# Optimization experiments

Hardware: AMD Instinct MI355X
Metric: run time of the kernel (lower is better)

Reference implementation:

```python
import jax, jax.numpy as jnp
import numpy as np

N_USERS = 200000
N_SPOTS = 50000
N_EDGES = 3200000
D = 64


def setup_inputs() -> dict:
    key = jax.random.key(0)
    k1, k2, k3, k4 = jax.random.split(key, 4)
    return {
        "user_x": jax.random.normal(k1, (N_USERS, D), dtype=jnp.float32),
        "spot_x": jax.random.normal(k2, (N_SPOTS, D), dtype=jnp.float32),
        "user_idx": jax.random.randint(k3, (N_EDGES,), 0, N_USERS, dtype=jnp.int32),
        "spot_idx": jax.random.randint(k4, (N_EDGES,), 0, N_SPOTS, dtype=jnp.int32),
    }


def reference(user_x, spot_x, user_idx, spot_idx):
    n_users, n_spots = user_x.shape[0], spot_x.shape[0]
    dtype = user_x.dtype
    ones = jnp.ones(user_idx.shape[0], dtype=dtype)
    # per-node degrees (counts of edge endpoints); isolated nodes get 1e-6
    user_div = jax.ops.segment_sum(ones, user_idx, num_segments=n_users)
    spot_div = jax.ops.segment_sum(ones, spot_idx, num_segments=n_spots)
    user_div = jnp.where(user_div == 0, jnp.asarray(1e-6, dtype), user_div)
    spot_div = jnp.where(spot_div == 0, jnp.asarray(1e-6, dtype), spot_div)
    inv_sqrt_user = jax.lax.rsqrt(user_div)  # [n_users]
    inv_sqrt_spot = jax.lax.rsqrt(spot_div)  # [n_spots]
    # gather + pre-normalize per-edge messages
    spot_msg = spot_x[spot_idx] * inv_sqrt_spot[spot_idx][:, None]  # [E, D]
    user_msg = user_x[user_idx] * inv_sqrt_user[user_idx][:, None]  # [E, D]
    # scatter-add into destination nodes, then post-normalize by dest degree
    spot_out = jax.ops.segment_sum(user_msg, spot_idx, num_segments=n_spots)
    user_out = jax.ops.segment_sum(spot_msg, user_idx, num_segments=n_users)
    spot_out = spot_out * inv_sqrt_spot[:, None]
    user_out = user_out * inv_sqrt_user[:, None]
    return (user_out, spot_out)
```

## Files before the change

### kernel.cpp

```cpp
#include <hip/hip_runtime.h>
#include <hip/hip_fp16.h>

#define DFEAT  64
#define BSH    7
#define BN     128
#define PBITS  18
#define PMASK  ((1u << PBITS) - 1)
#define NSPLIT 384
#define STR_U  2560
#define STR_S  9216

typedef float          __attribute__((ext_vector_type(4))) f32x4;
typedef unsigned short __attribute__((ext_vector_type(4))) u16x4;


__device__ __forceinline__ long long bucket_base(int b, int NB_U) {
    return (b < NB_U) ? (long long)b * STR_U
                      : (long long)NB_U * STR_U + (long long)(b - NB_U) * STR_S;
}

__global__ __launch_bounds__(256) void split_kernel(const int* __restrict__ uidx,
                                                    const int* __restrict__ sidx,
                                                    int* __restrict__ cursor,
                                                    unsigned int* __restrict__ staging,
                                                    int n_edges, int NB_U, int NB) {
    __shared__ int h[2048];
    __shared__ int rc[2048];
    for (int i = threadIdx.x; i < NB; i += 256) h[i] = 0;
    __syncthreads();
    int epb = (((n_edges + gridDim.x - 1) / gridDim.x) + 3) & ~3;
    int e0 = blockIdx.x * epb;
    int e1 = min(e0 + epb, n_edges);
    int len = e1 - e0; if (len < 0) len = 0;
    int nv = e0 + (len & ~3);
    for (int v = e0 + 4 * (int)threadIdx.x; v < nv; v += 1024) {
        int4 u = *(const int4*)(uidx + v);
        int4 s = *(const int4*)(sidx + v);
        atomicAdd(&h[u.x >> BSH], 1); atomicAdd(&h[u.y >> BSH], 1);
        atomicAdd(&h[u.z >> BSH], 1); atomicAdd(&h[u.w >> BSH], 1);
        atomicAdd(&h[NB_U + (s.x >> BSH)], 1); atomicAdd(&h[NB_U + (s.y >> BSH)], 1);
        atomicAdd(&h[NB_U + (s.z >> BSH)], 1); atomicAdd(&h[NB_U + (s.w >> BSH)], 1);
    }
    for (int e = nv + (int)threadIdx.x; e < e1; e += 256) {
        atomicAdd(&h[uidx[e] >> BSH], 1);
        atomicAdd(&h[NB_U + (sidx[e] >> BSH)], 1);
    }
    __syncthreads();
    for (int i = threadIdx.x; i < NB; i += 256) {
        int c = h[i];
        rc[i] = c ? (int)(bucket_base(i, NB_U) + atomicAdd(&cursor[i], c)) : 0;
    }
    __syncthreads();
    for (int v = e0 + 4 * (int)threadIdx.x; v < nv; v += 1024) {
        int4 u4 = *(const int4*)(uidx + v);
        int4 s4 = *(const int4*)(sidx + v);
#pragma unroll
        for (int k = 0; k < 4; ++k) {
            int u = ((const int*)&u4)[k];
            int s = ((const int*)&s4)[k];
            int pu = atomicAdd(&rc[u >> BSH], 1);
            staging[pu] = ((unsigned int)(u & (BN - 1)) << PBITS) | (unsigned int)s;
            int ps = atomicAdd(&rc[NB_U + (s >> BSH)], 1);
            staging[ps] = ((unsigned int)(s & (BN - 1)) << PBITS) | (unsigned int)u;
        }
    }
    for (int e = nv + (int)threadIdx.x; e < e1; e += 256) {
        int u = uidx[e], s = sidx[e];
        int pu = atomicAdd(&rc[u >> BSH], 1);
        staging[pu] = ((unsigned int)(u & (BN - 1)) << PBITS) | (unsigned int)s;
        int ps = atomicAdd(&rc[NB_U + (s >> BSH)], 1);
        staging[ps] = ((unsigned int)(s & (BN - 1)) << PBITS) | (unsigned int)u;
    }
}

template <int CAPN>
__global__ __launch_bounds__(256) void csr_build_inplace_t(
        unsigned int* __restrict__ staging,
        const int* __restrict__ cursor,
        int* __restrict__ start,
        int* __restrict__ cnt,
        float* __restrict__ isq,
        const float* __restrict__ ux,
        const float* __restrict__ sx,
        unsigned short* __restrict__ scaledH,
        int n_users, int n_spots,
        int NB_U, int b0) {
    __shared__ unsigned int buf[CAPN];
    __shared__ int hist[BN];
    __shared__ int scanbuf[BN];
    __shared__ int cur[BN];
    __shared__ float fisq[BN];
    int b = b0 + blockIdx.x, t = threadIdx.x;
    long long beg = bucket_base(b, NB_U);
    int len = cursor[b];
    if (len > CAPN) len = CAPN;
    if (t < BN) hist[t] = 0;
    __syncthreads();
    for (int i = t; i < len; i += 256) {
        unsigned int e = __builtin_nontemporal_load(&staging[beg + i]);
        buf[i] = e;
        atomicAdd(&hist[e >> PBITS], 1);
    }
    __syncthreads();
    if (t < BN) scanbuf[t] = hist[t];
    __syncthreads();
    for (int off = 1; off < BN; off <<= 1) {
        int v = (t >= off && t < BN) ? scanbuf[t - off] : 0;
        __syncthreads();
        if (t < BN) scanbuf[t] += v;
        __syncthreads();
    }
    bool ub = (b < NB_U);
    int node0 = (ub ? (b << BSH) : ((b - NB_U) << BSH));
    int lim   = ub ? n_users : n_spots;
    if (t < BN) {
        int excl = scanbuf[t] - hist[t];
        cur[t] = (int)beg + excl;
        int node = node0 + t;
        if (node < lim) {
            int gi = ub ? node : (n_users + node);
            start[gi] = (int)beg + excl;
            cnt[gi]   = hist[t];
            float d = hist[t] ? (float)hist[t] : 1e-6f;
            float is = rsqrtf(d);
            isq[gi]  = is;
            fisq[t]  = is;
        }
    }
    __syncthreads();
    for (int i = t; i < len; i += 256) {
        unsigned int e = buf[i];
        int pos = atomicAdd(&cur[e >> PBITS], 1);
        staging[pos] = e & PMASK;
    }
    const f32x4* __restrict__ xs4 = (const f32x4*)(ub ? ux : sx);
    u16x4* __restrict__ dst4 = (u16x4*)scaledH + ((long long)(ub ? node0 : n_users + node0) << 4);
#pragma unroll
    for (int k = 0; k < 8; ++k) {
        int idx4 = t + k * 256;
        int nl = idx4 >> 4;
        int node = node0 + nl;
        if (node < lim) {
            f32x4 v = __builtin_nontemporal_load(xs4 + ((long long)node << 4) + (idx4 & 15));
            float f = fisq[nl];
            u16x4 hh;
            hh.x = __half_as_ushort(__float2half(v.x * f));
            hh.y = __half_as_ushort(__float2half(v.y * f));
            hh.z = __half_as_ushort(__float2half(v.z * f));
            hh.w = __half_as_ushort(__float2half(v.w * f));
            dst4[((long long)nl << 4) + (idx4 & 15)] = hh;
        }
    }
}

template <int G>
__device__ __forceinline__ void gather_groupH(int j, int pv,
        const unsigned short* __restrict__ src, int lane,
        float& a0, float& a1, float& a2, float& a3) {
    unsigned short v[G];
#pragma unroll
    for (int k = 0; k < G; ++k) {
        int p = __builtin_amdgcn_readlane(pv, j + k);
        v[k] = src[(p << 6) + lane];
    }
    __builtin_amdgcn_sched_barrier(0);
#pragma unroll
    for (int k = 0; k < G; ++k) {
        float x = __half2float(__ushort_as_half(v[k]));
        if ((k & 3) == 0) a0 += x;
        else if ((k & 3) == 1) a1 += x;
        else if ((k & 3) == 2) a2 += x;
        else a3 += x;
    }
}

__global__ __launch_bounds__(256) void gather_h(
        const unsigned short* __restrict__ scaled,
        const float* __restrict__ isq,
        const int* __restrict__ start,
        const int* __restrict__ cnt,
        const int* __restrict__ csr,
        float* __restrict__ user_out,
        float* __restrict__ spot_out,
        int n_users, int n_spots) {
    int lane = (int)threadIdx.x & 63;
    int w = __builtin_amdgcn_readfirstlane((int)blockIdx.x * 4 + ((int)threadIdx.x >> 6));
    int A = n_users + n_spots;
    if (w >= A) return;
    bool ub = (w < n_users);
    const unsigned short* __restrict__ src =
        scaled + (ub ? ((long long)n_users << 6) : 0);
    int beg = __builtin_amdgcn_readfirstlane(start[w]);
    int end = beg + __builtin_amdgcn_readfirstlane(cnt[w]);
    float a0 = 0.f, a1 = 0.f, a2 = 0.f, a3 = 0.f;
    for (int i = beg; i < end; i += 64) {
        int n = end - i; if (n > 64) n = 64;
        int pv = 0;
        if (lane < n) pv = __builtin_nontemporal_load(&csr[i + lane]);
        int j = 0;
        for (; j + 16 <= n; j += 16)
            gather_groupH<16>(j, pv, src, lane, a0, a1, a2, a3);
        if (j + 8 <= n) { gather_groupH<8>(j, pv, src, lane, a0, a1, a2, a3); j += 8; }
        if (j + 4 <= n) { gather_groupH<4>(j, pv, src, lane, a0, a1, a2, a3); j += 4; }
        for (; j < n; ++j) {
            int p = __builtin_amdgcn_readlane(pv, j);
            a0 += __half2float(__ushort_as_half(src[(p << 6) + lane]));
        }
    }
    float r = ((a0 + a1) + (a2 + a3)) * isq[w];
    if (ub) __builtin_nontemporal_store(r, &user_out[((long long)w << 6) + lane]);
    else    __builtin_nontemporal_store(r, &spot_out[((long long)(w - n_users) << 6) + lane]);
}


__global__ void deg_kernel(const int* __restrict__ uidx,
                           const int* __restrict__ sidx,
                           unsigned int* __restrict__ udeg,
                           unsigned int* __restrict__ sdeg,
                           int n_edges) {
    int e = blockIdx.x * blockDim.x + threadIdx.x;
    if (e < n_edges) {
        atomicAdd(&udeg[uidx[e]], 1u);
        atomicAdd(&sdeg[sidx[e]], 1u);
    }
}

__global__ void rsqrt_kernel(unsigned int* __restrict__ deg_as_uint,
                             float* __restrict__ isq, int n) {
    int i = blockIdx.x * blockDim.x + threadIdx.x;
    if (i < n) {
        float d = (float)deg_as_uint[i];
        if (d == 0.0f) d = 1e-6f;
        isq[i] = rsqrtf(d);
    }
}

__global__ void scatter_kernel(const float* __restrict__ user_x,
                               const float* __restrict__ spot_x,
                               const int* __restrict__ uidx,
                               const int* __restrict__ sidx,
                               const float* __restrict__ isqu,
                               const float* __restrict__ isqs,
                               float* __restrict__ user_out,
                               float* __restrict__ spot_out,
                               int n_edges) {
    long long t = (long long)blockIdx.x * blockDim.x + threadIdx.x;
    int e = (int)(t >> 6);
    int lane = (int)(t & 63);
    if (e < n_edges) {
        int u = uidx[e];
        int s = sidx[e];
        float sv = spot_x[(long long)s * DFEAT + lane] * isqs[s];
        float uv = user_x[(long long)u * DFEAT + lane] * isqu[u];
        unsafeAtomicAdd(&user_out[(long long)u * DFEAT + lane], sv);
        unsafeAtomicAdd(&spot_out[(long long)s * DFEAT + lane], uv);
    }
}

__global__ void scale_kernel(float* __restrict__ user_out,
                             float* __restrict__ spot_out,
                             const float* __restrict__ isqu,
                             const float* __restrict__ isqs,
                             int n_users, int n_spots) {
    long long t = (long long)blockIdx.x * blockDim.x + threadIdx.x;
    long long total_u = (long long)n_users * DFEAT;
    long long total_s = (long long)n_spots * DFEAT;
    if (t < total_u) {
        user_out[t] *= isqu[t >> 6];
    } else if (t < total_u + total_s) {
        long long t2 = t - total_u;
        spot_out[t2] *= isqs[t2 >> 6];
    }
}


extern "C" void kernel_launch(void* const* d_in, const int* in_sizes, int n_in,
                              void* d_out, int out_size, void* d_ws, size_t ws_size,
                              hipStream_t stream) {
    const float* user_x = (const float*)d_in[0];
    const float* spot_x = (const float*)d_in[1];
    const int* uidx = (const int*)d_in[2];
    const int* sidx = (const int*)d_in[3];

    const int n_users = in_sizes[0] / DFEAT;
    const int n_spots = in_sizes[1] / DFEAT;
    const int n_edges = in_sizes[2];
    const int A = n_users + n_spots;

    float* user_out = (float*)d_out;
    float* spot_out = (float*)d_out + (long long)n_users * DFEAT;

    const int NB_U = (n_users + BN - 1) / BN;
    const int NB_S = (n_spots + BN - 1) / BN;
    const int NB = NB_U + NB_S;

    const long long SE = (long long)NB_U * STR_U + (long long)NB_S * STR_S;
    const long long off_start = NB;
    const long long off_cnt   = off_start + A;
    const long long off_isq   = off_cnt + A;
    const long long off_stg   = off_isq + A;
    const long long off_scl   = (off_stg + SE + 1) & ~1LL;
    const long long need = off_scl * 4 + (long long)A * DFEAT * 2;

    bool fits = NB <= 2048 &&
                n_users <= (1 << PBITS) && n_spots <= (1 << PBITS);

    if (fits && (long long)ws_size >= need) {
        int* cursor           = (int*)d_ws;
        int* start            = (int*)d_ws + off_start;
        int* cnt              = (int*)d_ws + off_cnt;
        float* isq            = (float*)d_ws + off_isq;
        unsigned int* staging = (unsigned int*)d_ws + off_stg;
        unsigned short* scaledH = (unsigned short*)((int*)d_ws + off_scl);

        hipMemsetAsync(cursor, 0, (size_t)NB * 4, stream);

        split_kernel<<<NSPLIT, 256, 0, stream>>>(uidx, sidx, cursor, staging,
                                                 n_edges, NB_U, NB);
        csr_build_inplace_t<STR_S><<<NB_S, 256, 0, stream>>>(
            staging, cursor, start, cnt, isq, user_x, spot_x, scaledH,
            n_users, n_spots, NB_U, NB_U);
        csr_build_inplace_t<STR_U><<<NB_U, 256, 0, stream>>>(
            staging, cursor, start, cnt, isq, user_x, spot_x, scaledH,
            n_users, n_spots, NB_U, 0);
        {
            long long total = (long long)A * 64;
            int blocks = (int)((total + 255) / 256);
            gather_h<<<blocks, 256, 0, stream>>>(
                scaledH, isq, start, cnt, (const int*)staging,
                user_out, spot_out, n_users, n_spots);
        }
    } else {
        float* isqu = (float*)d_ws;
        float* isqs = isqu + n_users;
        unsigned int* udeg = (unsigned int*)isqu;
        unsigned int* sdeg = (unsigned int*)isqs;

        hipMemsetAsync(d_out, 0, (size_t)out_size * sizeof(float), stream);
        hipMemsetAsync(d_ws, 0, (size_t)A * sizeof(unsigned int), stream);

        {
            int blocks = (n_edges + 255) / 256;
            deg_kernel<<<blocks, 256, 0, stream>>>(uidx, sidx, udeg, sdeg, n_edges);
        }
        {
            int blocks = (A + 255) / 256;
            rsqrt_kernel<<<blocks, 256, 0, stream>>>((unsigned int*)d_ws, (float*)d_ws, A);
        }
        {
            long long total = (long long)n_edges * 64;
            int blocks = (int)((total + 255) / 256);
            scatter_kernel<<<blocks, 256, 0, stream>>>(
                user_x, spot_x, uidx, sidx, isqu, isqs, user_out, spot_out, n_edges);
        }
        {
            long long total = (long long)A * 64;
            int blocks = (int)((total + 255) / 256);
            scale_kernel<<<blocks, 256, 0, stream>>>(
                user_out, spot_out, isqu, isqs, n_users, n_spots);
        }
    }
}
```

Before: 429.5 us.

## Shrink spot buckets to 32 nodes and sub-sort neighbors by coarse index bits

Spot buckets now hold 32 nodes instead of 128, so every bucket uses one uniform stride and the large 9216-entry shared buffer for spot buckets goes away. The sort key inside each bucket also carries high bits of the neighbor index (1 bit for user rows, 3 bits for spot rows), which orders each node's adjacency list into coarse neighbor ranges. The aim is higher occupancy in the CSR build and better gather locality in the later aggregation. The cost is more buckets, more split-histogram shared memory (MAXNB) and a 256-bin scan per block.

```diff
diff --git a/kernel.cpp b/kernel.cpp
--- a/kernel.cpp
+++ b/kernel.cpp
@@ -2,30 +2,26 @@
 #include <hip/hip_fp16.h>
 
 #define DFEAT  64
-#define BSH    7
-#define BN     128
+#define BSH_U  7
+#define BSH_S  5
 #define PBITS  18
 #define PMASK  ((1u << PBITS) - 1)
 #define NSPLIT 384
-#define STR_U  2560
-#define STR_S  9216
+#define STR    2560
+#define MAXNB  3328
 
 typedef float          __attribute__((ext_vector_type(4))) f32x4;
 typedef unsigned short __attribute__((ext_vector_type(4))) u16x4;
 
 
-__device__ __forceinline__ long long bucket_base(int b, int NB_U) {
-    return (b < NB_U) ? (long long)b * STR_U
-                      : (long long)NB_U * STR_U + (long long)(b - NB_U) * STR_S;
-}
-
 __global__ __launch_bounds__(256) void split_kernel(const int* __restrict__ uidx,
                                                     const int* __restrict__ sidx,
-                                                    int* __restrict__ cursor,
+                                                    int* __restrict__ bcursor,
                                                     unsigned int* __restrict__ staging,
-                                                    int n_edges, int NB_U, int NB) {
-    __shared__ int h[2048];
-    __shared__ int rc[2048];
+                                                    int n_edges, int NB_U, int NB,
+                                                    int shs, int shu) {
+    __shared__ int h[MAXNB];
+    __shared__ int rc[MAXNB];
     for (int i = threadIdx.x; i < NB; i += 256) h[i] = 0;
     __syncthreads();
     int epb = (((n_edges + gridDim.x - 1) / gridDim.x) + 3) & ~3;
@@ -36,19 +32,19 @@
     for (int v = e0 + 4 * (int)threadIdx.x; v < nv; v += 1024) {
         int4 u = *(const int4*)(uidx + v);
         int4 s = *(const int4*)(sidx + v);
-        atomicAdd(&h[u.x >> BSH], 1); atomicAdd(&h[u.y >> BSH], 1);
-        atomicAdd(&h[u.z >> BSH], 1); atomicAdd(&h[u.w >> BSH], 1);
-        atomicAdd(&h[NB_U + (s.x >> BSH)], 1); atomicAdd(&h[NB_U + (s.y >> BSH)], 1);
-        atomicAdd(&h[NB_U + (s.z >> BSH)], 1); atomicAdd(&h[NB_U + (s.w >> BSH)], 1);
+        atomicAdd(&h[u.x >> BSH_U], 1); atomicAdd(&h[u.y >> BSH_U], 1);
+        atomicAdd(&h[u.z >> BSH_U], 1); atomicAdd(&h[u.w >> BSH_U], 1);
+        atomicAdd(&h[NB_U + (s.x >> BSH_S)], 1); atomicAdd(&h[NB_U + (s.y >> BSH_S)], 1);
+        atomicAdd(&h[NB_U + (s.z >> BSH_S)], 1); atomicAdd(&h[NB_U + (s.w >> BSH_S)], 1);
     }
     for (int e = nv + (int)threadIdx.x; e < e1; e += 256) {
-        atomicAdd(&h[uidx[e] >> BSH], 1);
-        atomicAdd(&h[NB_U + (sidx[e] >> BSH)], 1);
+        atomicAdd(&h[uidx[e] >> BSH_U], 1);
+        atomicAdd(&h[NB_U + (sidx[e] >> BSH_S)], 1);
     }
     __syncthreads();
     for (int i = threadIdx.x; i < NB; i += 256) {
         int c = h[i];
-        rc[i] = c ? (int)(bucket_base(i, NB_U) + atomicAdd(&cursor[i], c)) : 0;
+        rc[i] = c ? (int)((long long)i * STR + atomicAdd(&bcursor[i], c)) : 0;
     }
     __syncthreads();
     for (int v = e0 + 4 * (int)threadIdx.x; v < nv; v += 1024) {
@@ -58,43 +54,46 @@
         for (int k = 0; k < 4; ++k) {
             int u = ((const int*)&u4)[k];
             int s = ((const int*)&s4)[k];
-            int pu = atomicAdd(&rc[u >> BSH], 1);
-            staging[pu] = ((unsigned int)(u & (BN - 1)) << PBITS) | (unsigned int)s;
-            int ps = atomicAdd(&rc[NB_U + (s >> BSH)], 1);
-            staging[ps] = ((unsigned int)(s & (BN - 1)) << PBITS) | (unsigned int)u;
+            unsigned int ku = ((unsigned int)(u & 127) << 1) | (unsigned int)(s >> shs);
+            int pu = atomicAdd(&rc[u >> BSH_U], 1);
+            staging[pu] = (ku << PBITS) | (unsigned int)s;
+            unsigned int ks = ((unsigned int)(s & 31) << 3) | (unsigned int)(u >> shu);
+            int ps = atomicAdd(&rc[NB_U + (s >> BSH_S)], 1);
+            staging[ps] = (ks << PBITS) | (unsigned int)u;
         }
     }
     for (int e = nv + (int)threadIdx.x; e < e1; e += 256) {
         int u = uidx[e], s = sidx[e];
-        int pu = atomicAdd(&rc[u >> BSH], 1);
-        staging[pu] = ((unsigned int)(u & (BN - 1)) << PBITS) | (unsigned int)s;
-        int ps = atomicAdd(&rc[NB_U + (s >> BSH)], 1);
-        staging[ps] = ((unsigned int)(s & (BN - 1)) << PBITS) | (unsigned int)u;
-    }
-}
-
-template <int CAPN>
-__global__ __launch_bounds__(256) void csr_build_inplace_t(
+        unsigned int ku = ((unsigned int)(u & 127) << 1) | (unsigned int)(s >> shs);
+        int pu = atomicAdd(&rc[u >> BSH_U], 1);
+        staging[pu] = (ku << PBITS) | (unsigned int)s;
+        unsigned int ks = ((unsigned int)(s & 31) << 3) | (unsigned int)(u >> shu);
+        int ps = atomicAdd(&rc[NB_U + (s >> BSH_S)], 1);
+        staging[ps] = (ks << PBITS) | (unsigned int)u;
+    }
+}
+
+template <int RB, int BNODES, bool UB>
+__global__ __launch_bounds__(256) void csr_build_t(
         unsigned int* __restrict__ staging,
-        const int* __restrict__ cursor,
+        const int* __restrict__ bcursor,
         int* __restrict__ start,
         int* __restrict__ cnt,
         float* __restrict__ isq,
         const float* __restrict__ ux,
         const float* __restrict__ sx,
         unsigned short* __restrict__ scaledH,
-        int n_users, int n_spots,
-        int NB_U, int b0) {
-    __shared__ unsigned int buf[CAPN];
-    __shared__ int hist[BN];
-    __shared__ int scanbuf[BN];
-    __shared__ int cur[BN];
-    __shared__ float fisq[BN];
+        int n_users, int n_spots, int NB_U, int b0) {
+    __shared__ unsigned int buf[STR];
+    __shared__ int hist[256];
+    __shared__ int scanbuf[256];
+    __shared__ int cur[256];
+    __shared__ float fisq[BNODES];
+    constexpr int NSH = (BNODES == 128) ? 7 : 5;
     int b = b0 + blockIdx.x, t = threadIdx.x;
-    long long beg = bucket_base(b, NB_U);
-    int len = cursor[b];
-    if (len > CAPN) len = CAPN;
-    if (t < BN) hist[t] = 0;
+    long long beg = (long long)b * STR;
+    int len = bcursor[b]; if (len > STR) len = STR;
+    hist[t] = 0;
     __syncthreads();
     for (int i = t; i < len; i += 256) {
         unsigned int e = __builtin_nontemporal_load(&staging[beg + i]);
@@ -102,30 +101,32 @@
         atomicAdd(&hist[e >> PBITS], 1);
     }
     __syncthreads();
-    if (t < BN) scanbuf[t] = hist[t];
-    __syncthreads();
-    for (int off = 1; off < BN; off <<= 1) {
-        int v = (t >= off && t < BN) ? scanbuf[t - off] : 0;
+    scanbuf[t] = hist[t];
+    __syncthreads();
+    for (int off = 1; off < 256; off <<= 1) {
+        int v = (t >= off) ? scanbuf[t - off] : 0;
         __syncthreads();
-        if (t < BN) scanbuf[t] += v;
+        scanbuf[t] += v;
         __syncthreads();
     }
-    bool ub = (b < NB_U);
-    int node0 = (ub ? (b << BSH) : ((b - NB_U) << BSH));
-    int lim   = ub ? n_users : n_spots;
-    if (t < BN) {
-        int excl = scanbuf[t] - hist[t];
-        cur[t] = (int)beg + excl;
+    cur[t] = (int)beg + scanbuf[t] - hist[t];
+    int node0 = UB ? (b << NSH) : ((b - NB_U) << NSH);
+    int lim   = UB ? n_users : n_spots;
+    if (t < BNODES) {
+        int fb = t << RB, lb = ((t + 1) << RB) - 1;
+        int excl0 = scanbuf[fb] - hist[fb];
+        int c = scanbuf[lb] - excl0;
         int node = node0 + t;
+        float is = 0.f;
         if (node < lim) {
-            int gi = ub ? node : (n_users + node);
-            start[gi] = (int)beg + excl;
-            cnt[gi]   = hist[t];
-            float d = hist[t] ? (float)hist[t] : 1e-6f;
-            float is = rsqrtf(d);
-            isq[gi]  = is;
-            fisq[t]  = is;
-        }
+            int gi = UB ? node : (n_users + node);
+            start[gi] = (int)beg + excl0;
+            cnt[gi]   = c;
+            float d = c ? (float)c : 1e-6f;
+            is = rsqrtf(d);
+            isq[gi] = is;
+        }
+        fisq[t] = is;
     }
     __syncthreads();
     for (int i = t; i < len; i += 256) {
@@ -133,10 +134,12 @@
         int pos = atomicAdd(&cur[e >> PBITS], 1);
         staging[pos] = e & PMASK;
     }
-    const f32x4* __restrict__ xs4 = (const f32x4*)(ub ? ux : sx);
-    u16x4* __restrict__ dst4 = (u16x4*)scaledH + ((long long)(ub ? node0 : n_users + node0) << 4);
+    const f32x4* __restrict__ xs4 = (const f32x4*)(UB ? ux : sx);
+    long long gbase = UB ? (long long)node0 : (long long)(n_users + node0);
+    u16x4* __restrict__ dst4 = (u16x4*)scaledH + (gbase << 4);
+    constexpr int ITER = (BNODES << 4) / 256;
 #pragma unroll
-    for (int k = 0; k < 8; ++k) {
+    for (int k = 0; k < ITER; ++k) {
         int idx4 = t + k * 256;
         int nl = idx4 >> 4;
         int node = node0 + nl;
@@ -290,11 +293,14 @@
     float* user_out = (float*)d_out;
     float* spot_out = (float*)d_out + (long long)n_users * DFEAT;
 
-    const int NB_U = (n_users + BN - 1) / BN;
-    const int NB_S = (n_spots + BN - 1) / BN;
+    const int NB_U = (n_users + 127) >> BSH_U;
+    const int NB_S = (n_spots + 31) >> BSH_S;
     const int NB = NB_U + NB_S;
 
-    const long long SE = (long long)NB_U * STR_U + (long long)NB_S * STR_S;
+    int shs = 0; while (((n_spots - 1) >> shs) > 1) shs++;
+    int shu = 0; while (((n_users - 1) >> shu) > 7) shu++;
+
+    const long long SE = (long long)NB * STR;
     const long long off_start = NB;
     const long long off_cnt   = off_start + A;
     const long long off_isq   = off_cnt + A;
@@ -302,26 +308,26 @@
     const long long off_scl   = (off_stg + SE + 1) & ~1LL;
     const long long need = off_scl * 4 + (long long)A * DFEAT * 2;
 
-    bool fits = NB <= 2048 &&
+    bool fits = NB <= MAXNB &&
                 n_users <= (1 << PBITS) && n_spots <= (1 << PBITS);
 
     if (fits && (long long)ws_size >= need) {
-        int* cursor           = (int*)d_ws;
-        int* start            = (int*)d_ws + off_start;
-        int* cnt              = (int*)d_ws + off_cnt;
-        float* isq            = (float*)d_ws + off_isq;
-        unsigned int* staging = (unsigned int*)d_ws + off_stg;
+        int* bcursor            = (int*)d_ws;
+        int* start              = (int*)d_ws + off_start;
+        int* cnt                = (int*)d_ws + off_cnt;
+        float* isq              = (float*)d_ws + off_isq;
+        unsigned int* staging   = (unsigned int*)d_ws + off_stg;
         unsigned short* scaledH = (unsigned short*)((int*)d_ws + off_scl);
 
-        hipMemsetAsync(cursor, 0, (size_t)NB * 4, stream);
-
-        split_kernel<<<NSPLIT, 256, 0, stream>>>(uidx, sidx, cursor, staging,
-                                                 n_edges, NB_U, NB);
-        csr_build_inplace_t<STR_S><<<NB_S, 256, 0, stream>>>(
-            staging, cursor, start, cnt, isq, user_x, spot_x, scaledH,
+        hipMemsetAsync(bcursor, 0, (size_t)NB * 4, stream);
+
+        split_kernel<<<NSPLIT, 256, 0, stream>>>(uidx, sidx, bcursor, staging,
+                                                 n_edges, NB_U, NB, shs, shu);
+        csr_build_t<3, 32, false><<<NB_S, 256, 0, stream>>>(
+            staging, bcursor, start, cnt, isq, user_x, spot_x, scaledH,
             n_users, n_spots, NB_U, NB_U);
-        csr_build_inplace_t<STR_U><<<NB_U, 256, 0, stream>>>(
-            staging, cursor, start, cnt, isq, user_x, spot_x, scaledH,
+        csr_build_t<1, 128, true><<<NB_U, 256, 0, stream>>>(
+            staging, bcursor, start, cnt, isq, user_x, spot_x, scaledH,
             n_users, n_spots, NB_U, 0);
         {
             long long total = (long long)A * 64;
```

Result: no change. 428.1 us (-0.3%).
